# Kernel tuning notes

Hardware: AMD Instinct MI355X
Metric: run time of the kernel (lower is better)

The kernel has to match this reference:

```python
import jax, jax.numpy as jnp
import numpy as np

N, K = 100000, 16
IN, H, OUT = 128, 256, 128
EPS = 1e-5
NEG_SLOPE = 0.2


def _bn(x, gamma, beta):
    # training-mode BatchNorm1d: biased batch stats over dim 0
    m = jnp.mean(x, axis=0)
    v = jnp.mean(jnp.square(x - m), axis=0)
    return (x - m) * jax.lax.rsqrt(v + EPS) * gamma + beta


def _layer(x, W, b, gamma, beta):
    x = x @ W.T + b
    x = jnp.where(x > 0, x, NEG_SLOPE * x)  # LeakyReLU(0.2)
    return _bn(x, gamma, beta)


def setup_inputs() -> dict:
    key = jax.random.key(0)
    ks = jax.random.split(key, 8)
    inp = {
        "input_features": jax.random.normal(ks[0], (N, IN), dtype=jnp.float32),
        "neigh_idx": jax.random.randint(ks[1], (N * K,), 0, N, dtype=jnp.int64 if jax.config.jax_enable_x64 else jnp.int32),
        "prob_retained": 1,
        "W1": jax.random.normal(ks[2], (H, IN), dtype=jnp.float32) * 0.05,
        "b1": jnp.zeros((H,), dtype=jnp.float32),
        "g1": jnp.ones((H,), dtype=jnp.float32),
        "beta1": jnp.zeros((H,), dtype=jnp.float32),
        "W2": jax.random.normal(ks[3], (H, H), dtype=jnp.float32) * 0.05,
        "b2": jnp.zeros((H,), dtype=jnp.float32),
        "g2": jnp.ones((H,), dtype=jnp.float32),
        "beta2": jnp.zeros((H,), dtype=jnp.float32),
        "W3": jax.random.normal(ks[4], (OUT, H), dtype=jnp.float32) * 0.05,
        "b3": jnp.zeros((OUT,), dtype=jnp.float32),
        "g3": jnp.ones((OUT,), dtype=jnp.float32),
        "beta3": jnp.zeros((OUT,), dtype=jnp.float32),
    }
    return inp


def reference(input_features, neigh_idx, prob_retained,
              W1, b1, g1, beta1, W2, b2, g2, beta2, W3, b3, g3, beta3):
    # MLP (BN branch, len(x) > 1)
    f = _layer(input_features, W1, b1, g1, beta1)   # [N, H]
    f = _layer(f, W2, b2, g2, beta2)                # [N, H]
    f = _layer(f, W3, b3, g3, beta3)                # [N, OUT]
    # per-node neighbor mean: index_select + mean, fixed degree K
    node_update = f[neigh_idx].reshape(N, K, OUT).mean(axis=1)  # [N, OUT]
    return (node_update, f)
```

## Files before the change

kernel.cpp:

```cpp
#include <hip/hip_runtime.h>
#include <hip/hip_bf16.h>

typedef __bf16 bf16x8 __attribute__((ext_vector_type(8)));
typedef __bf16 bf16x2 __attribute__((ext_vector_type(2)));
typedef float f32x4 __attribute__((ext_vector_type(4)));

#define NROWS 100000
#define NSTRIPS 6250
#define EPS 1e-5f
#define SLOPE 0.2f

__device__ __forceinline__ bf16x8 cvt8(const float* s) {
    float4 x0 = *(const float4*)s, x1 = *(const float4*)(s + 4);
    bf16x8 o;
    o[0] = (__bf16)x0.x; o[1] = (__bf16)x0.y; o[2] = (__bf16)x0.z; o[3] = (__bf16)x0.w;
    o[4] = (__bf16)x1.x; o[5] = (__bf16)x1.y; o[6] = (__bf16)x1.z; o[7] = (__bf16)x1.w;
    return o;
}

template <int KT, int NI, bool F32IN>
__global__ __launch_bounds__(256, 2)
void gemm_stream(const __bf16* __restrict__ A, const float* __restrict__ A32,
                 const __bf16* __restrict__ W, const float* __restrict__ W32,
                 const float* __restrict__ bias, __bf16* __restrict__ Y,
                 float* __restrict__ sum, float* __restrict__ sumsq)
{
    constexpr int KS = KT / 32;
    constexpr int NCOLS = NI * 64;
    const int wave = threadIdx.x >> 6, lane = threadIdx.x & 63;
    const int quad = lane >> 4, l16 = lane & 15;
    const int c0 = wave * (NI * 16);

    bf16x8 bfrag[NI][KS];
    float bcol[NI];
    #pragma unroll
    for (int ni = 0; ni < NI; ++ni) {
        int col = c0 + ni * 16 + l16;
        bcol[ni] = bias[col];
        #pragma unroll
        for (int ks = 0; ks < KS; ++ks) {
            int k = ks * 32 + quad * 8;
            if constexpr (F32IN) bfrag[ni][ks] = cvt8(W32 + (size_t)col * KT + k);
            else                 bfrag[ni][ks] = *(const bf16x8*)(W + (size_t)col * KT + k);
        }
    }

    float csum[NI] = {}, csq[NI] = {};

    for (int s = blockIdx.x; s < NSTRIPS; s += gridDim.x) {
        int row0 = s * 16;
        bf16x8 afrag[KS];
        #pragma unroll
        for (int ks = 0; ks < KS; ++ks) {
            int k = ks * 32 + quad * 8;
            if constexpr (F32IN) afrag[ks] = cvt8(A32 + (size_t)(row0 + l16) * KT + k);
            else                 afrag[ks] = *(const bf16x8*)(A + (size_t)(row0 + l16) * KT + k);
        }
        f32x4 acc[NI] = {};
        #pragma unroll
        for (int ks = 0; ks < KS; ++ks)
            #pragma unroll
            for (int ni = 0; ni < NI; ++ni)
                acc[ni] = __builtin_amdgcn_mfma_f32_16x16x32_bf16(
                    afrag[ks], bfrag[ni][ks], acc[ni], 0, 0, 0);

        #pragma unroll
        for (int ni = 0; ni < NI; ++ni) {
            int col = c0 + ni * 16 + l16;
            #pragma unroll
            for (int r = 0; r < 4; ++r) {
                float y = acc[ni][r] + bcol[ni];
                y = (y > 0.f) ? y : SLOPE * y;
                Y[(size_t)(row0 + quad * 4 + r) * NCOLS + col] = (__bf16)y;
                csum[ni] += y;
                csq[ni]  += y * y;
            }
        }
    }

    #pragma unroll
    for (int ni = 0; ni < NI; ++ni) {
        float s = csum[ni], q = csq[ni];
        s += __shfl_xor(s, 16); s += __shfl_xor(s, 32);
        q += __shfl_xor(q, 16); q += __shfl_xor(q, 32);
        if (quad == 0) {
            int col = c0 + ni * 16 + l16;
            atomicAdd(&sum[col], s);
            atomicAdd(&sumsq[col], q);
        }
    }
}

__global__ void stats_k(const float* __restrict__ sum, const float* __restrict__ sumsq,
                        const float* __restrict__ g, const float* __restrict__ beta,
                        float* __restrict__ s, float* __restrict__ t,
                        int Ncols, float invN)
{
    int c = blockIdx.x * blockDim.x + threadIdx.x;
    if (c < Ncols) {
        float m = sum[c] * invN;
        float v = sumsq[c] * invN - m * m;
        float sc = g[c] * rsqrtf(v + EPS);
        s[c] = sc;
        t[c] = beta[c] - m * sc;
    }
}

__global__ void fold_k(const float* __restrict__ W, const float* __restrict__ b,
                       const float* __restrict__ s, const float* __restrict__ t,
                       __bf16* __restrict__ Wf, float* __restrict__ bf_, int K)
{
    int n = blockIdx.x;
    int lane = threadIdx.x;
    float dot = 0.f;
    for (int k = lane; k < K; k += 64) {
        float w = W[(size_t)n * K + k];
        Wf[(size_t)n * K + k] = (__bf16)(w * s[k]);
        dot += w * t[k];
    }
    #pragma unroll
    for (int off = 32; off; off >>= 1) dot += __shfl_down(dot, off);
    if (lane == 0) bf_[n] = b[n] + dot;
}

__global__ void bn_apply(const __bf16* __restrict__ Y, const float* __restrict__ s,
                         const float* __restrict__ t, float* __restrict__ F, long n8)
{
    long i = blockIdx.x * (long)blockDim.x + threadIdx.x;
    if (i >= n8) return;
    bf16x8 v = *(const bf16x8*)(Y + i * 8);
    int c0 = (int)((i * 8) & 127);
    float4 f0, f1;
    f0.x = (float)v[0] * s[c0 + 0] + t[c0 + 0];
    f0.y = (float)v[1] * s[c0 + 1] + t[c0 + 1];
    f0.z = (float)v[2] * s[c0 + 2] + t[c0 + 2];
    f0.w = (float)v[3] * s[c0 + 3] + t[c0 + 3];
    f1.x = (float)v[4] * s[c0 + 4] + t[c0 + 4];
    f1.y = (float)v[5] * s[c0 + 5] + t[c0 + 5];
    f1.z = (float)v[6] * s[c0 + 6] + t[c0 + 6];
    f1.w = (float)v[7] * s[c0 + 7] + t[c0 + 7];
    *(float4*)(F + i * 8) = f0;
    *(float4*)(F + i * 8 + 4) = f1;
}

__global__ __launch_bounds__(256)
void gather_mean_bn(const __bf16* __restrict__ Y3, const int* __restrict__ idx,
                    const float* __restrict__ s3, const float* __restrict__ t3,
                    float* __restrict__ out, int N)
{
    int row = blockIdx.x * 4 + (threadIdx.x >> 6);
    if (row >= N) return;
    int lane = threadIdx.x & 63;
    const int* ib = idx + (size_t)row * 16;
    float a0 = 0.f, a1 = 0.f;
    #pragma unroll
    for (int k = 0; k < 16; ++k) {
        int j = ib[k];
        bf16x2 v = *(const bf16x2*)(Y3 + (size_t)j * 128 + lane * 2);
        a0 += (float)v[0];
        a1 += (float)v[1];
    }
    float2 sc = *(const float2*)(s3 + lane * 2);
    float2 tc = *(const float2*)(t3 + lane * 2);
    float2 o;
    o.x = a0 * 0.0625f * sc.x + tc.x;
    o.y = a1 * 0.0625f * sc.y + tc.y;
    *(float2*)(out + (size_t)row * 128 + lane * 2) = o;
}

extern "C" void kernel_launch(void* const* d_in, const int* in_sizes, int n_in,
                              void* d_out, int out_size, void* d_ws, size_t ws_size,
                              hipStream_t stream)
{
    const float* X   = (const float*)d_in[0];
    const int*   idx = (const int*)d_in[1];
    const float* W1  = (const float*)d_in[3];
    const float* b1  = (const float*)d_in[4];
    const float* g1  = (const float*)d_in[5];
    const float* be1 = (const float*)d_in[6];
    const float* W2  = (const float*)d_in[7];
    const float* b2  = (const float*)d_in[8];
    const float* g2  = (const float*)d_in[9];
    const float* be2 = (const float*)d_in[10];
    const float* W3  = (const float*)d_in[11];
    const float* b3  = (const float*)d_in[12];
    const float* g3  = (const float*)d_in[13];
    const float* be3 = (const float*)d_in[14];

    char* ws = (char*)d_ws;
    float* sum1 = (float*)(ws + 0);
    float* sq1  = (float*)(ws + 1024);
    float* sum2 = (float*)(ws + 2048);
    float* sq2  = (float*)(ws + 3072);
    float* sum3 = (float*)(ws + 4096);
    float* sq3  = (float*)(ws + 4608);
    float* s1   = (float*)(ws + 5120);
    float* t1   = (float*)(ws + 6144);
    float* s2   = (float*)(ws + 7168);
    float* t2   = (float*)(ws + 8192);
    float* s3   = (float*)(ws + 9216);
    float* t3   = (float*)(ws + 9728);
    float* b2f  = (float*)(ws + 10240);
    float* b3f  = (float*)(ws + 11264);
    __bf16* W2f = (__bf16*)(ws + 13312);
    __bf16* W3f = (__bf16*)(ws + 144384);
    __bf16* Y1  = (__bf16*)(ws + (1 << 20));
    __bf16* Y2  = (__bf16*)(ws + (1 << 20) + 51200000);
    __bf16* Y3  = Y1;

    float* out_nu = (float*)d_out;
    float* F      = out_nu + (size_t)NROWS * 128;

    const float invN = 1.0f / (float)NROWS;
    const dim3 blk(256);
    const int GB = 512;

    hipMemsetAsync(d_ws, 0, 5120, stream);

    gemm_stream<128, 4, true><<<GB, blk, 0, stream>>>(
        nullptr, X, nullptr, W1, b1, Y1, sum1, sq1);
    stats_k<<<1, 256, 0, stream>>>(sum1, sq1, g1, be1, s1, t1, 256, invN);
    fold_k<<<256, 64, 0, stream>>>(W2, b2, s1, t1, W2f, b2f, 256);

    gemm_stream<256, 4, false><<<GB, blk, 0, stream>>>(
        Y1, nullptr, W2f, nullptr, b2f, Y2, sum2, sq2);
    stats_k<<<1, 256, 0, stream>>>(sum2, sq2, g2, be2, s2, t2, 256, invN);
    fold_k<<<128, 64, 0, stream>>>(W3, b3, s2, t2, W3f, b3f, 256);

    gemm_stream<256, 2, false><<<GB, blk, 0, stream>>>(
        Y2, nullptr, W3f, nullptr, b3f, Y3, sum3, sq3);
    stats_k<<<1, 128, 0, stream>>>(sum3, sq3, g3, be3, s3, t3, 128, invN);

    bn_apply<<<6250, 256, 0, stream>>>(Y3, s3, t3, F, (long)NROWS * 128 / 8);
    gather_mean_bn<<<25000, 256, 0, stream>>>(Y3, idx, s3, t3, out_nu, NROWS);
}
```

Baseline: 365.5 us.

## Split GEMM columns across grid, fuse BN stats into fold and bn_apply into gather

The GEMM kernel now gives each block only 128 output columns (NI fixed at 2) and uses a 2D grid, which cuts the per-thread weight-fragment registers and allows higher occupancy through the WPE launch bound. The stats and fold kernels are merged into one fold_bn kernel, and the bn_apply pass is folded into the gather kernel, removing several launches and one separate read of Y3. The trade-off is that the A operand is now loaded twice, once per column half, for layers 1 and 2.

```diff
diff --git a/kernel.cpp b/kernel.cpp
--- a/kernel.cpp
+++ b/kernel.cpp
@@ -18,18 +18,18 @@
     return o;
 }
 
-template <int KT, int NI, bool F32IN>
-__global__ __launch_bounds__(256, 2)
+template <int KT, int NROWSTRIDE, bool F32IN, int WPE>
+__global__ __launch_bounds__(256, WPE)
 void gemm_stream(const __bf16* __restrict__ A, const float* __restrict__ A32,
                  const __bf16* __restrict__ W, const float* __restrict__ W32,
                  const float* __restrict__ bias, __bf16* __restrict__ Y,
                  float* __restrict__ sum, float* __restrict__ sumsq)
 {
     constexpr int KS = KT / 32;
-    constexpr int NCOLS = NI * 64;
+    constexpr int NI = 2;
     const int wave = threadIdx.x >> 6, lane = threadIdx.x & 63;
     const int quad = lane >> 4, l16 = lane & 15;
-    const int c0 = wave * (NI * 16);
+    const int c0 = blockIdx.y * 128 + wave * 32;
 
     bf16x8 bfrag[NI][KS];
     float bcol[NI];
@@ -71,7 +71,7 @@
             for (int r = 0; r < 4; ++r) {
                 float y = acc[ni][r] + bcol[ni];
                 y = (y > 0.f) ? y : SLOPE * y;
-                Y[(size_t)(row0 + quad * 4 + r) * NCOLS + col] = (__bf16)y;
+                Y[(size_t)(row0 + quad * 4 + r) * NROWSTRIDE + col] = (__bf16)y;
                 csum[ni] += y;
                 csq[ni]  += y * y;
             }
@@ -91,6 +91,39 @@
     }
 }
 
+__global__ __launch_bounds__(256)
+void fold_bn(const float* __restrict__ sum, const float* __restrict__ sumsq,
+             const float* __restrict__ g, const float* __restrict__ beta,
+             const float* __restrict__ W, const float* __restrict__ b,
+             __bf16* __restrict__ Wf, float* __restrict__ bf_,
+             int Nrows, float invN)
+{
+    __shared__ float sS[256], sT[256];
+    const int t = threadIdx.x;
+    {
+        float m = sum[t] * invN;
+        float v = sumsq[t] * invN - m * m;
+        float sc = g[t] * rsqrtf(v + EPS);
+        sS[t] = sc;
+        sT[t] = beta[t] - m * sc;
+    }
+    __syncthreads();
+    const int wave = t >> 6, lane = t & 63;
+    for (int n = blockIdx.x * 4 + wave; n < Nrows; n += gridDim.x * 4) {
+        float dot = 0.f;
+        #pragma unroll
+        for (int kk = 0; kk < 4; ++kk) {
+            int k = kk * 64 + lane;
+            float w = W[(size_t)n * 256 + k];
+            Wf[(size_t)n * 256 + k] = (__bf16)(w * sS[k]);
+            dot += w * sT[k];
+        }
+        #pragma unroll
+        for (int off = 32; off; off >>= 1) dot += __shfl_down(dot, off);
+        if (lane == 0) bf_[n] = b[n] + dot;
+    }
+}
+
 __global__ void stats_k(const float* __restrict__ sum, const float* __restrict__ sumsq,
                         const float* __restrict__ g, const float* __restrict__ beta,
                         float* __restrict__ s, float* __restrict__ t,
@@ -106,51 +139,17 @@
     }
 }
 
-__global__ void fold_k(const float* __restrict__ W, const float* __restrict__ b,
-                       const float* __restrict__ s, const float* __restrict__ t,
-                       __bf16* __restrict__ Wf, float* __restrict__ bf_, int K)
-{
-    int n = blockIdx.x;
-    int lane = threadIdx.x;
-    float dot = 0.f;
-    for (int k = lane; k < K; k += 64) {
-        float w = W[(size_t)n * K + k];
-        Wf[(size_t)n * K + k] = (__bf16)(w * s[k]);
-        dot += w * t[k];
-    }
-    #pragma unroll
-    for (int off = 32; off; off >>= 1) dot += __shfl_down(dot, off);
-    if (lane == 0) bf_[n] = b[n] + dot;
-}
-
-__global__ void bn_apply(const __bf16* __restrict__ Y, const float* __restrict__ s,
-                         const float* __restrict__ t, float* __restrict__ F, long n8)
-{
-    long i = blockIdx.x * (long)blockDim.x + threadIdx.x;
-    if (i >= n8) return;
-    bf16x8 v = *(const bf16x8*)(Y + i * 8);
-    int c0 = (int)((i * 8) & 127);
-    float4 f0, f1;
-    f0.x = (float)v[0] * s[c0 + 0] + t[c0 + 0];
-    f0.y = (float)v[1] * s[c0 + 1] + t[c0 + 1];
-    f0.z = (float)v[2] * s[c0 + 2] + t[c0 + 2];
-    f0.w = (float)v[3] * s[c0 + 3] + t[c0 + 3];
-    f1.x = (float)v[4] * s[c0 + 4] + t[c0 + 4];
-    f1.y = (float)v[5] * s[c0 + 5] + t[c0 + 5];
-    f1.z = (float)v[6] * s[c0 + 6] + t[c0 + 6];
-    f1.w = (float)v[7] * s[c0 + 7] + t[c0 + 7];
-    *(float4*)(F + i * 8) = f0;
-    *(float4*)(F + i * 8 + 4) = f1;
-}
-
 __global__ __launch_bounds__(256)
-void gather_mean_bn(const __bf16* __restrict__ Y3, const int* __restrict__ idx,
-                    const float* __restrict__ s3, const float* __restrict__ t3,
-                    float* __restrict__ out, int N)
+void finalize(const __bf16* __restrict__ Y3, const int* __restrict__ idx,
+              const float* __restrict__ s3, const float* __restrict__ t3,
+              float* __restrict__ out, float* __restrict__ F, int N)
 {
     int row = blockIdx.x * 4 + (threadIdx.x >> 6);
     if (row >= N) return;
     int lane = threadIdx.x & 63;
+    float2 sc = *(const float2*)(s3 + lane * 2);
+    float2 tc = *(const float2*)(t3 + lane * 2);
+
     const int* ib = idx + (size_t)row * 16;
     float a0 = 0.f, a1 = 0.f;
     #pragma unroll
@@ -160,8 +159,13 @@
         a0 += (float)v[0];
         a1 += (float)v[1];
     }
-    float2 sc = *(const float2*)(s3 + lane * 2);
-    float2 tc = *(const float2*)(t3 + lane * 2);
+
+    bf16x2 mv = *(const bf16x2*)(Y3 + (size_t)row * 128 + lane * 2);
+    float2 fo;
+    fo.x = (float)mv[0] * sc.x + tc.x;
+    fo.y = (float)mv[1] * sc.y + tc.y;
+    *(float2*)(F + (size_t)row * 128 + lane * 2) = fo;
+
     float2 o;
     o.x = a0 * 0.0625f * sc.x + tc.x;
     o.y = a1 * 0.0625f * sc.y + tc.y;
@@ -194,10 +198,6 @@
     float* sq2  = (float*)(ws + 3072);
     float* sum3 = (float*)(ws + 4096);
     float* sq3  = (float*)(ws + 4608);
-    float* s1   = (float*)(ws + 5120);
-    float* t1   = (float*)(ws + 6144);
-    float* s2   = (float*)(ws + 7168);
-    float* t2   = (float*)(ws + 8192);
     float* s3   = (float*)(ws + 9216);
     float* t3   = (float*)(ws + 9728);
     float* b2f  = (float*)(ws + 10240);
@@ -213,24 +213,20 @@
 
     const float invN = 1.0f / (float)NROWS;
     const dim3 blk(256);
-    const int GB = 512;
 
     hipMemsetAsync(d_ws, 0, 5120, stream);
 
-    gemm_stream<128, 4, true><<<GB, blk, 0, stream>>>(
+    gemm_stream<128, 256, true, 4><<<dim3(512, 2), blk, 0, stream>>>(
         nullptr, X, nullptr, W1, b1, Y1, sum1, sq1);
-    stats_k<<<1, 256, 0, stream>>>(sum1, sq1, g1, be1, s1, t1, 256, invN);
-    fold_k<<<256, 64, 0, stream>>>(W2, b2, s1, t1, W2f, b2f, 256);
-
-    gemm_stream<256, 4, false><<<GB, blk, 0, stream>>>(
+    fold_bn<<<64, blk, 0, stream>>>(sum1, sq1, g1, be1, W2, b2, W2f, b2f, 256, invN);
+
+    gemm_stream<256, 256, false, 3><<<dim3(384, 2), blk, 0, stream>>>(
         Y1, nullptr, W2f, nullptr, b2f, Y2, sum2, sq2);
-    stats_k<<<1, 256, 0, stream>>>(sum2, sq2, g2, be2, s2, t2, 256, invN);
-    fold_k<<<128, 64, 0, stream>>>(W3, b3, s2, t2, W3f, b3f, 256);
-
-    gemm_stream<256, 2, false><<<GB, blk, 0, stream>>>(
+    fold_bn<<<32, blk, 0, stream>>>(sum2, sq2, g2, be2, W3, b3, W3f, b3f, 128, invN);
+
+    gemm_stream<256, 128, false, 3><<<dim3(768, 1), blk, 0, stream>>>(
         Y2, nullptr, W3f, nullptr, b3f, Y3, sum3, sq3);
     stats_k<<<1, 128, 0, stream>>>(sum3, sq3, g3, be3, s3, t3, 128, invN);
 
-    bn_apply<<<6250, 256, 0, stream>>>(Y3, s3, t3, F, (long)NROWS * 128 / 8);
-    gather_mean_bn<<<25000, 256, 0, stream>>>(Y3, idx, s3, t3, out_nu, NROWS);
-}
+    finalize<<<25000, blk, 0, stream>>>(Y3, idx, s3, t3, out_nu, F, NROWS);
+}
```

Result: slower. 383.6 us (+5.0%).
